# Performance work log

Hardware: AMD Instinct MI355X
Metric: run time of the kernel (lower is better)

Reference implementation:

```python
import jax, jax.numpy as jnp
import numpy as np


def setup_inputs() -> dict:
    key = jax.random.key(0)
    k_w, k_xi, k_u = jax.random.split(key, 3)
    N, d, M, L, B = 4096, 512, 256, 16, 1024
    W = 2 * L + 1  # window width = 33
    # xavier-normal-ish scale for weight (fan_in=d, fan_out=M*W per torch xavier on last dim pairs)
    w_scale = (2.0 / (W + d)) ** 0.5
    xi_scale = (2.0 / (M + N + 2 * L)) ** 0.5
    weight = jax.random.normal(k_w, (M, W, d), dtype=jnp.float32) * w_scale
    bias = jnp.zeros((M, W, 1), dtype=jnp.float32)
    xi = jax.random.normal(k_xi, (M, N + 2 * L), dtype=jnp.float32) * xi_scale
    u = jax.random.normal(k_u, (B, d), dtype=jnp.float32)
    return {"u": u, "weight": weight, "bias": bias, "xi": xi}


def reference(u, weight, bias, xi):
    # weight: [M, W, d], bias: [M, W, 1], xi: [M, N + W - 1], u: [B, d]
    M, W, d = weight.shape
    N = xi.shape[1] - (W - 1)
    # first_step: G[m, j, b] = sigmoid(sum_k weight[m,j,k] * u[b,k] + bias[m,j])
    G = jax.nn.sigmoid(jnp.einsum('mjd,bd->mjb', weight, u) + bias)  # [M, W, B]
    # im2col-style unfold of xi into overlapping windows, replacing the N-step Python loop
    idx = jnp.arange(N)[:, None] + jnp.arange(W)[None, :]  # [N, W]
    Xw = xi[:, idx]  # [M, N, W]
    # out[n, b] = sum_{m, j} xi[m, n+j] * G[m, j, b]  == torch.cat of iter_prod rows
    return jnp.einsum('mnj,mjb->nb', Xw, G)  # [N, B]
```

## Files before the change

### kernel.cpp

```cpp
#include <hip/hip_runtime.h>
#include <hip/hip_bf16.h>

typedef __attribute__((ext_vector_type(8))) short bf16x8;
typedef __attribute__((ext_vector_type(4))) float f32x4;
typedef unsigned int u32;
typedef unsigned short u16;

#define XI_ROW 4128
#define KP     8448
#define NB     1024
#define NN     4096
#define DDIM   512

__device__ __forceinline__ u16 f2bf(float f) {
  union { float f; unsigned u; } c; c.f = f;
  return (u16)((c.u + 0x7FFFu + ((c.u >> 16) & 1u)) >> 16);
}
__device__ __forceinline__ float bf2f(u16 h) {
  union { u32 u; float f; } c; c.u = ((u32)h) << 16; return c.f;
}
__device__ __forceinline__ u32 pk2bf(float a, float b) {
  return (u32)f2bf(a) | ((u32)f2bf(b) << 16);
}
__device__ __forceinline__ void gld16(const u16* g, u16* l) {
  __builtin_amdgcn_global_load_lds(
      (const __attribute__((address_space(1))) u32*)(const void*)g,
      (__attribute__((address_space(3))) u32*)(void*)l, 16, 0, 0);
}

#define BAR() __builtin_amdgcn_s_barrier()
#define LGKM0() asm volatile("s_waitcnt lgkmcnt(0)" ::: "memory")
#define LGKM8() asm volatile("s_waitcnt lgkmcnt(8)" ::: "memory")
#define WAITVM(N) asm volatile("s_waitcnt vmcnt(" #N ")" ::: "memory")
#define SCHED0() __builtin_amdgcn_sched_barrier(0)

__global__ __launch_bounds__(256) void k_prep(
    const float* __restrict__ w, const float* __restrict__ u,
    const float* __restrict__ xi, u16* __restrict__ Wbf,
    u16* __restrict__ Ubf, u16* __restrict__ xiT) {
  __shared__ u16 tile[32][33];
  const int bx = blockIdx.x, t = threadIdx.x;
  if (bx < 4224) {
    int kp = bx * 2 + (t >> 7), tl = t & 127;
    int m = kp & 255, j = kp >> 8;
    float4 v = ((const float4*)(w + (size_t)(m * 33 + j) * DDIM))[tl];
    ((uint2*)(Wbf + (size_t)kp * DDIM))[tl] =
        make_uint2(pk2bf(v.x, v.y), pk2bf(v.z, v.w));
  } else if (bx < 4736) {
    int b = (bx - 4224) * 2 + (t >> 7), tl = t & 127;
    float4 v = ((const float4*)(u + (size_t)b * DDIM))[tl];
    ((uint2*)(Ubf + (size_t)b * DDIM))[tl] =
        make_uint2(pk2bf(v.x, v.y), pk2bf(v.z, v.w));
  } else {
    int bx2 = bx - 4736;
    int cblk = bx2 % 129, mblk = bx2 / 129;
    int c0 = cblk * 32, m0 = mblk * 32;
    int tx = t & 31, ty = t >> 5;
#pragma unroll
    for (int i = 0; i < 4; ++i)
      tile[ty + i * 8][tx] = f2bf(xi[(size_t)(m0 + ty + i * 8) * XI_ROW + c0 + tx]);
    __syncthreads();
#pragma unroll
    for (int i = 0; i < 4; ++i)
      xiT[(size_t)(c0 + ty + i * 8) * 256 + m0 + tx] = tile[tx][ty + i * 8];
  }
}

template<int KSTEPS, int AS, int BS>
__device__ __forceinline__ void gemm_pipeline(
    const u16* __restrict__ aSrc, const u16* __restrict__ bSrc,
    u16* As0, u16* As1, u16* Bl0, u16* Bl1,
    int wid, int wr, int wc, int rl, int kg, int rl7,
    f32x4 (&acc)[4][4]) {

  auto stage = [&](u16* Ab, u16* Bb, int kk) {
#pragma unroll
    for (int i = 0; i < 4; ++i)
      gld16(aSrc + (size_t)i * 8 * AS + kk, &Ab[(wid * 4 + i) * 512]);
#pragma unroll
    for (int i = 0; i < 4; ++i)
      gld16(bSrc + (size_t)i * 8 * BS + kk, &Bb[(wid * 4 + i) * 512]);
  };
  auto compute = [&](const u16* Ab, const u16* Bb) {
#pragma unroll
    for (int kh = 0; kh < 2; ++kh) {
      bf16x8 af[4], bfv[4];
#pragma unroll
      for (int fm = 0; fm < 4; ++fm)
        af[fm] = *(const bf16x8*)&Ab[(wr * 64 + fm * 16 + rl) * 64 +
                                     (((kh * 4 + kg) ^ rl7) * 8)];
#pragma unroll
      for (int fn = 0; fn < 4; ++fn)
        bfv[fn] = *(const bf16x8*)&Bb[(wc * 64 + fn * 16 + rl) * 64 +
                                      (((kh * 4 + kg) ^ rl7) * 8)];
      __builtin_amdgcn_s_setprio(1);
#pragma unroll
      for (int fm = 0; fm < 4; ++fm)
#pragma unroll
        for (int fn = 0; fn < 4; ++fn)
          acc[fm][fn] = __builtin_amdgcn_mfma_f32_16x16x32_bf16(
              af[fm], bfv[fn], acc[fm][fn], 0, 0, 0);
      __builtin_amdgcn_s_setprio(0);
    }
  };

  stage(As0, Bl0, 0);
  WAITVM(0);
  BAR();
#pragma unroll 1
  for (int ts = 0; ts < KSTEPS - 2; ts += 2) {
    stage(As1, Bl1, (ts + 1) * 64);
    WAITVM(8);
    BAR();
    compute(As0, Bl0);
    BAR();
    stage(As0, Bl0, (ts + 2) * 64);
    WAITVM(8);
    BAR();
    compute(As1, Bl1);
    BAR();
  }
  stage(As1, Bl1, (KSTEPS - 1) * 64);
  WAITVM(8);
  BAR();
  compute(As0, Bl0);
  BAR();
  WAITVM(0);
  BAR();
  compute(As1, Bl1);
}

__global__ __launch_bounds__(256) void k_gemm1(
    const u16* __restrict__ Wbf, const u16* __restrict__ Ubf,
    const float* __restrict__ Bsrc, u16* __restrict__ Gt) {
  __shared__ u16 lds1[32768];
  u16* As0 = lds1;
  u16* As1 = lds1 + 8192;
  u16* Bl0 = lds1 + 16384;
  u16* Bl1 = lds1 + 24576;
  const int r0 = blockIdx.x * 128;
  const int b0 = blockIdx.y * 128;
  const int t = threadIdx.x, lane = t & 63, wid = t >> 6;
  const int wr = wid >> 1, wc = wid & 1;
  const int rl = lane & 15, kg = lane >> 4, rl7 = rl & 7;
  const int lr = lane >> 3, lc = (lane & 7) ^ (lr & 7);
  const u16* aSrc = Wbf + (size_t)(r0 + wid * 32 + lr) * DDIM + lc * 8;
  const u16* bSrc = Ubf + (size_t)(b0 + wid * 32 + lr) * DDIM + lc * 8;

  f32x4 acc[4][4] = {};
  gemm_pipeline<8, DDIM, DDIM>(aSrc, bSrc, As0, As1, Bl0, Bl1,
                               wid, wr, wc, rl, kg, rl7, acc);

  __syncthreads();
  u16* Lt = lds1;
#pragma unroll
  for (int fm = 0; fm < 4; ++fm) {
    int kloc = wr * 64 + fm * 16 + kg * 4;
    int kbase = r0 + kloc;
    float b4[4];
#pragma unroll
    for (int r = 0; r < 4; ++r) {
      int kk = kbase + r;
      b4[r] = Bsrc[(kk & 255) * 33 + (kk >> 8)];
    }
#pragma unroll
    for (int fn = 0; fn < 4; ++fn) {
      int bloc = wc * 64 + fn * 16 + rl;
      u16 o[4];
#pragma unroll
      for (int r = 0; r < 4; ++r) {
        float x = acc[fm][fn][r] + b4[r];
        o[r] = f2bf(1.0f / (1.0f + __expf(-x)));
      }
      *(uint2*)&Lt[bloc * 136 + kloc] =
          make_uint2((u32)o[0] | ((u32)o[1] << 16),
                     (u32)o[2] | ((u32)o[3] << 16));
    }
  }
  __syncthreads();
  const int bl = t >> 4, j = t & 15;
#pragma unroll
  for (int p = 0; p < 8; ++p) {
    int bloc = p * 16 + bl;
    uint4 v = *(const uint4*)&Lt[bloc * 136 + j * 8];
    *(uint4*)(Gt + (size_t)(b0 + bloc) * KP + r0 + j * 8) = v;
  }
}

__global__ __launch_bounds__(512, 2) void k_gemm2(
    const u16* __restrict__ xiT, const u16* __restrict__ Gt,
    float* __restrict__ Out, u16* __restrict__ Part, int allbf) {
  __shared__ u16 lds[65536];
  const int lid = blockIdx.x;
  const int b0 = (lid & 3) * 256;
  const int ks = (lid >> 2) & 3;
  const int n0 = (lid >> 4) * 256;
  const int kOff = (ks < 2) ? ks * 2176 : 4352 + (ks - 2) * 2048;
  const int nt = (ks < 2) ? 34 : 32;

  const int t = threadIdx.x, lane = t & 63, wid = t >> 6;
  const int wr = wid >> 2, wc = wid & 3;
  const int rl = lane & 15, kg = lane >> 4, rl7 = rl & 7;
  const int sr = lane >> 3;
  const int sc = (lane & 7) ^ sr;

  const u16* aS = xiT + (size_t)(n0 + wid * 16 + sr) * 256 + kOff + sc * 8;
  const u16* bS = Gt  + (size_t)(b0 + wid * 16 + sr) * KP  + kOff + sc * 8;

  f32x4 acc[8][4] = {};
  bf16x8 af[8], b01[4], b23[4];

  auto stA = [&](int tile, int half, int buf) {
    u16* d = lds + (buf * 4 + half) * 8192 + wid * 1024;
    const u16* s = aS + (size_t)half * 32768 + (size_t)tile * 64;
    gld16(s, d);
    gld16(s + 2048, d + 512);
  };
  auto stB = [&](int tile, int half, int buf) {
    u16* d = lds + (buf * 4 + 2 + half) * 8192 + wid * 1024;
    const u16* s = bS + (size_t)half * 128 * KP + (size_t)tile * 64;
    gld16(s, d);
    gld16(s + (size_t)8 * KP, d + 512);
  };
  auto rdA = [&](int buf, int sub) {
    const u16* p = lds + (buf * 4 + wr) * 8192;
#pragma unroll
    for (int q = 0; q < 4; ++q)
#pragma unroll
      for (int kh = 0; kh < 2; ++kh)
        af[q * 2 + kh] = *(const bf16x8*)
            &p[((sub * 4 + q) * 16 + rl) * 64 + (((kh * 4 + kg) ^ rl7) * 8)];
  };
  auto rdB = [&](int buf, int sub, bf16x8 (&bq)[4]) {
    const u16* p = lds + (buf * 4 + 2 + (wc >> 1)) * 8192;
#pragma unroll
    for (int q = 0; q < 2; ++q)
#pragma unroll
      for (int kh = 0; kh < 2; ++kh)
        bq[q * 2 + kh] = *(const bf16x8*)
            &p[((wc & 1) * 64 + (sub * 2 + q) * 16 + rl) * 64 +
               (((kh * 4 + kg) ^ rl7) * 8)];
  };
  auto mm = [&](int sm, int sn, bf16x8 (&bq)[4]) {
    __builtin_amdgcn_s_setprio(1);
#pragma unroll
    for (int q = 0; q < 4; ++q)
#pragma unroll
      for (int p = 0; p < 2; ++p)
#pragma unroll
        for (int kh = 0; kh < 2; ++kh)
          acc[sm * 4 + q][sn * 2 + p] = __builtin_amdgcn_mfma_f32_16x16x32_bf16(
              af[q * 2 + kh], bq[p * 2 + kh], acc[sm * 4 + q][sn * 2 + p], 0, 0, 0);
    __builtin_amdgcn_s_setprio(0);
  };

  auto runIter = [&](int T, bool s2, bool s3) {
    rdA(0, 0); rdB(0, 0, b01);
    if (s2 || true) {}
    stA(T + 1, 0, 1); stA(T + 1, 1, 1);
    LGKM8(); SCHED0(); BAR(); LGKM0(); SCHED0(); mm(0, 0, b01);
    rdB(0, 1, b23);
    SCHED0(); BAR(); LGKM0(); SCHED0(); mm(0, 1, b23);
    rdA(0, 1);
    SCHED0(); BAR(); LGKM0(); SCHED0(); mm(1, 0, b01);
    if (s2) { stB(T + 2, 0, 0); stB(T + 2, 1, 0); WAITVM(4); }
    else    { WAITVM(0); }
    SCHED0(); BAR(); SCHED0(); mm(1, 1, b23);
    rdA(1, 0); rdB(1, 0, b01);
    if (s2) { stA(T + 2, 0, 0); stA(T + 2, 1, 0); }
    LGKM8(); SCHED0(); BAR(); LGKM0(); SCHED0(); mm(0, 0, b01);
    rdB(1, 1, b23);
    SCHED0(); BAR(); LGKM0(); SCHED0(); mm(0, 1, b23);
    rdA(1, 1); if (s3) stB(T + 3, 0, 1);
    SCHED0(); BAR(); LGKM0(); SCHED0(); mm(1, 0, b01);
    if (s3) stB(T + 3, 1, 1);
    if (s2) WAITVM(4);
    SCHED0(); BAR(); SCHED0(); mm(1, 1, b23);
  };

  stA(0, 0, 0); stA(0, 1, 0); stB(0, 0, 0); stB(0, 1, 0);
  stB(1, 0, 1); stB(1, 1, 1);
  WAITVM(4);
  BAR();

  const int nIter = nt >> 1;
#pragma unroll 1
  for (int it = 0; it < nIter - 1; ++it) runIter(it * 2, true, true);
  runIter((nIter - 1) * 2, false, false);

  if (!allbf && ks == 0) {
#pragma unroll
    for (int fm = 0; fm < 8; ++fm)
#pragma unroll
      for (int fn = 0; fn < 4; ++fn) {
        int n = n0 + wr * 128 + fm * 16 + kg * 4;
        int b = b0 + wc * 64 + fn * 16 + rl;
#pragma unroll
        for (int r = 0; r < 4; ++r)
          Out[(size_t)(n + r) * NB + b] = acc[fm][fn][r];
      }
  } else {
    int slot = allbf ? ks : (ks - 1);
    u16* P = Part + (size_t)slot * (NN * NB);
#pragma unroll
    for (int fm = 0; fm < 8; ++fm)
#pragma unroll
      for (int fn = 0; fn < 4; ++fn) {
        int n = n0 + wr * 128 + fm * 16 + kg * 4;
        int b = b0 + wc * 64 + fn * 16 + rl;
#pragma unroll
        for (int r = 0; r < 4; ++r)
          P[(size_t)(n + r) * NB + b] = f2bf(acc[fm][fn][r]);
      }
  }
}

__global__ __launch_bounds__(256) void k_reduce(float* __restrict__ Out,
                                                const u16* __restrict__ Part,
                                                int allbf) {
  size_t i = (size_t)blockIdx.x * 256 + threadIdx.x;
  float4 a;
  int np;
  if (allbf) { a = make_float4(0.f, 0.f, 0.f, 0.f); np = 4; }
  else       { a = ((const float4*)Out)[i];          np = 3; }
  for (int p = 0; p < np; ++p) {
    ushort4 v = ((const ushort4*)(Part + (size_t)p * (NN * NB)))[i];
    a.x += bf2f(v.x); a.y += bf2f(v.y); a.z += bf2f(v.z); a.w += bf2f(v.w);
  }
  ((float4*)Out)[i] = a;
}

extern "C" void kernel_launch(void* const* d_in, const int* in_sizes, int n_in,
                              void* d_out, int out_size, void* d_ws, size_t ws_size,
                              hipStream_t stream) {
  const float* u  = (const float*)d_in[0];
  const float* w  = (const float*)d_in[1];
  const float* bs = (const float*)d_in[2];
  const float* xi = (const float*)d_in[3];
  float* out = (float*)d_out;

  u16* xiT  = (u16*)d_ws;
  u16* Gt   = (u16*)((char*)d_ws + 2113536);
  u16* Wbf  = (u16*)((char*)d_ws + 19415040);
  u16* Ubf  = (u16*)((char*)d_ws + 28065792);
  u16* Part = (u16*)((char*)d_ws + 19415040);
  const int allbf = (ws_size >= 52969472ull) ? 1 : 0;

  k_prep<<<5768, 256, 0, stream>>>(w, u, xi, Wbf, Ubf, xiT);
  k_gemm1<<<dim3(66, 8), 256, 0, stream>>>(Wbf, Ubf, bs, Gt);
  k_gemm2<<<256, 512, 0, stream>>>(xiT, Gt, out, Part, allbf);
  k_reduce<<<4096, 256, 0, stream>>>(out, Part, allbf);
}
```

Baseline: 99.56 us.

## Double-buffer A fragments in registers to overlap LDS reads with MFMA

```diff
diff --git a/kernel.cpp b/kernel.cpp
--- a/kernel.cpp
+++ b/kernel.cpp
@@ -29,8 +29,7 @@
 }
 
 #define BAR() __builtin_amdgcn_s_barrier()
-#define LGKM0() asm volatile("s_waitcnt lgkmcnt(0)" ::: "memory")
-#define LGKM8() asm volatile("s_waitcnt lgkmcnt(8)" ::: "memory")
+#define LGKMC(N) asm volatile("s_waitcnt lgkmcnt(" #N ")" ::: "memory")
 #define WAITVM(N) asm volatile("s_waitcnt vmcnt(" #N ")" ::: "memory")
 #define SCHED0() __builtin_amdgcn_sched_barrier(0)
 
@@ -208,7 +207,7 @@
   const u16* bS = Gt  + (size_t)(b0 + wid * 16 + sr) * KP  + kOff + sc * 8;
 
   f32x4 acc[8][4] = {};
-  bf16x8 af[8], b01[4], b23[4];
+  bf16x8 afA[8], afB[8], b01[4], b23[4];
 
   auto stA = [&](int tile, int half, int buf) {
     u16* d = lds + (buf * 4 + half) * 8192 + wid * 1024;
@@ -222,7 +221,7 @@
     gld16(s, d);
     gld16(s + (size_t)8 * KP, d + 512);
   };
-  auto rdA = [&](int buf, int sub) {
+  auto rdA = [&](bf16x8 (&af)[8], int buf, int sub) {
     const u16* p = lds + (buf * 4 + wr) * 8192;
 #pragma unroll
     for (int q = 0; q < 4; ++q)
@@ -241,7 +240,7 @@
             &p[((wc & 1) * 64 + (sub * 2 + q) * 16 + rl) * 64 +
                (((kh * 4 + kg) ^ rl7) * 8)];
   };
-  auto mm = [&](int sm, int sn, bf16x8 (&bq)[4]) {
+  auto mm = [&](bf16x8 (&af)[8], int sm, int sn, bf16x8 (&bq)[4]) {
     __builtin_amdgcn_s_setprio(1);
 #pragma unroll
     for (int q = 0; q < 4; ++q)
@@ -255,33 +254,42 @@
   };
 
   auto runIter = [&](int T, bool s2, bool s3) {
-    rdA(0, 0); rdB(0, 0, b01);
-    if (s2 || true) {}
     stA(T + 1, 0, 1); stA(T + 1, 1, 1);
-    LGKM8(); SCHED0(); BAR(); LGKM0(); SCHED0(); mm(0, 0, b01);
+    SCHED0(); BAR();
     rdB(0, 1, b23);
-    SCHED0(); BAR(); LGKM0(); SCHED0(); mm(0, 1, b23);
-    rdA(0, 1);
-    SCHED0(); BAR(); LGKM0(); SCHED0(); mm(1, 0, b01);
+    LGKMC(4); SCHED0(); mm(afA, 0, 0, b01);
+    SCHED0(); BAR();
+    rdA(afB, 0, 1);
+    LGKMC(8); SCHED0(); mm(afA, 0, 1, b23);
+    SCHED0(); BAR();
+    LGKMC(0); SCHED0(); mm(afB, 1, 0, b01);
     if (s2) { stB(T + 2, 0, 0); stB(T + 2, 1, 0); WAITVM(4); }
     else    { WAITVM(0); }
-    SCHED0(); BAR(); SCHED0(); mm(1, 1, b23);
-    rdA(1, 0); rdB(1, 0, b01);
+    SCHED0(); BAR();
+    rdA(afA, 1, 0); rdB(1, 0, b01);
+    SCHED0(); mm(afB, 1, 1, b23);
     if (s2) { stA(T + 2, 0, 0); stA(T + 2, 1, 0); }
-    LGKM8(); SCHED0(); BAR(); LGKM0(); SCHED0(); mm(0, 0, b01);
+    SCHED0(); BAR();
     rdB(1, 1, b23);
-    SCHED0(); BAR(); LGKM0(); SCHED0(); mm(0, 1, b23);
-    rdA(1, 1); if (s3) stB(T + 3, 0, 1);
-    SCHED0(); BAR(); LGKM0(); SCHED0(); mm(1, 0, b01);
+    LGKMC(4); SCHED0(); mm(afA, 0, 0, b01);
+    SCHED0(); BAR();
+    rdA(afB, 1, 1);
+    LGKMC(8); SCHED0(); mm(afA, 0, 1, b23);
+    if (s3) stB(T + 3, 0, 1);
+    SCHED0(); BAR();
+    LGKMC(0); SCHED0(); mm(afB, 1, 0, b01);
     if (s3) stB(T + 3, 1, 1);
     if (s2) WAITVM(4);
-    SCHED0(); BAR(); SCHED0(); mm(1, 1, b23);
+    SCHED0(); BAR();
+    if (s2) { rdA(afA, 0, 0); rdB(0, 0, b01); }
+    SCHED0(); mm(afB, 1, 1, b23);
   };
 
   stA(0, 0, 0); stA(0, 1, 0); stB(0, 0, 0); stB(0, 1, 0);
   stB(1, 0, 1); stB(1, 1, 1);
   WAITVM(4);
   BAR();
+  rdA(afA, 0, 0); rdB(0, 0, b01);
 
   const int nIter = nt >> 1;
 #pragma unroll 1
```

Result: slower. 115.5 us (+16.1%).
